# Kernel tuning notes

Measured on AMD Instinct MI355X. Metric: run time of the kernel, lower is better.

## Reference

```python
import jax, jax.numpy as jnp
import numpy as np

WINDOW_SIZES = (2, 4, 8)
HIDDEN = 32


def setup_inputs() -> dict:
    key = jax.random.key(0)
    ks = jax.random.split(key, 8)
    B, H, L = 4, 16, 1024
    S = len(WINDOW_SIZES)
    inp = {
        "attn_1": jax.random.uniform(ks[0], (B, H, L, L), dtype=jnp.float32),
        "attn_2": jax.random.uniform(ks[1], (B, H, L, L), dtype=jnp.float32),
        # gate MLP params, stacked over scales: Linear(8->32), Linear(32->16), Linear(16->1)
        "W1": jax.random.normal(ks[2], (S, HIDDEN, 8), dtype=jnp.float32) * 0.2,
        "b1": jnp.zeros((S, HIDDEN), dtype=jnp.float32),
        "W2": jax.random.normal(ks[3], (S, HIDDEN // 2, HIDDEN), dtype=jnp.float32) * 0.2,
        "b2": jnp.zeros((S, HIDDEN // 2), dtype=jnp.float32),
        "W3": jax.random.normal(ks[4], (S, 1, HIDDEN // 2), dtype=jnp.float32) * 0.2,
        "b3": jnp.zeros((S, 1), dtype=jnp.float32),
        "scale_weights": jnp.ones((S,), dtype=jnp.float32) / S,
    }
    return inp


def _window_stats(attn, ws):
    # attn: [B,H,L,L]; L % ws == 0 -> all windows are full-size (no edge merge)
    B, H, L, _ = attn.shape
    nw = L // ws
    x = attn.reshape(B, H, nw, ws, L)
    mean = x.mean(axis=-1).mean(axis=-1)                 # [B,H,nw]
    std = jnp.std(x, axis=-1, ddof=1).mean(axis=-1)      # torch.std is unbiased
    mx = x.max(axis=-1).mean(axis=-1)
    mn = x.min(axis=-1).mean(axis=-1)
    return jnp.stack([mean, std, mx, mn], axis=-1)        # [B,H,nw,4]


def reference(attn_1, attn_2, W1, b1, W2, b2, W3, b3, scale_weights):
    B, H, L, _ = attn_1.shape
    alphas = []
    for s, ws in enumerate(WINDOW_SIZES):
        g = jnp.concatenate([_window_stats(attn_1, ws), _window_stats(attn_2, ws)], axis=-1)  # [B,H,nw,8]
        h = jax.nn.relu(jnp.einsum('bhnf,of->bhno', g, W1[s]) + b1[s])
        h = jax.nn.relu(jnp.einsum('bhnf,of->bhno', h, W2[s]) + b2[s])
        a = jax.nn.sigmoid(jnp.einsum('bhnf,of->bhno', h, W3[s]) + b3[s])  # [B,H,nw,1]
        # expand per-window alpha to per-frame: repeat ws times (nw*ws == L)
        a_exp = jnp.repeat(a[..., 0], ws, axis=-1)[..., None]  # [B,H,L,1]
        alphas.append(a_exp)
    w = jax.nn.softmax(scale_weights)                     # all scales valid (max ws <= L)
    alpha_stacked = jnp.stack(alphas, axis=-1)            # [B,H,L,1,S]
    alpha_final = (alpha_stacked * w.reshape(1, 1, 1, 1, -1)).sum(axis=-1)
    return alpha_final
```

## Files before the change

kernel.cpp:

```cpp
#include <hip/hip_runtime.h>
#include <math.h>

#define L_DIM 1024
#define BH 64
#define ROWS_PER_TENSOR (BH * L_DIM)

typedef float floatx4 __attribute__((ext_vector_type(4)));

__global__ __launch_bounds__(256) void row_stats_kernel(
    const float* __restrict__ a1, const float* __restrict__ a2,
    float4* __restrict__ stats)
{
    const int wave = (blockIdx.x << 2) | (threadIdx.x >> 6);
    const int lane = threadIdx.x & 63;
    const int t = wave >> 16;
    const int r = wave & (ROWS_PER_TENSOR - 1);
    const float* __restrict__ src = t ? a2 : a1;
    const floatx4* __restrict__ rowp = (const floatx4*)(src + (size_t)r * L_DIM);

    float s = 0.f, sq = 0.f, mx = -INFINITY, mn = INFINITY;
#pragma unroll
    for (int c = 0; c < 4; ++c) {
        floatx4 v = __builtin_nontemporal_load(&rowp[(c << 6) + lane]);
        s  += v.x + v.y + v.z + v.w;
        sq += v.x * v.x + v.y * v.y + v.z * v.z + v.w * v.w;
        mx = fmaxf(mx, fmaxf(fmaxf(v.x, v.y), fmaxf(v.z, v.w)));
        mn = fminf(mn, fminf(fminf(v.x, v.y), fminf(v.z, v.w)));
    }
#pragma unroll
    for (int off = 32; off > 0; off >>= 1) {
        s  += __shfl_xor(s,  off, 64);
        sq += __shfl_xor(sq, off, 64);
        mx = fmaxf(mx, __shfl_xor(mx, off, 64));
        mn = fminf(mn, __shfl_xor(mn, off, 64));
    }
    if (lane == 0) {
        const float invL = 1.0f / (float)L_DIM;
        float mean = s * invL;
        float var  = (sq - s * s * invL) * (1.0f / (float)(L_DIM - 1));
        var = fmaxf(var, 0.f);
        float4 o;
        o.x = mean; o.y = sqrtf(var); o.z = mx; o.w = mn;
        stats[wave] = o;
    }
}

__global__ __launch_bounds__(256) void gate_kernel(
    const float4* __restrict__ stats,
    const float* __restrict__ W1, const float* __restrict__ b1,
    const float* __restrict__ W2, const float* __restrict__ b2,
    const float* __restrict__ W3, const float* __restrict__ b3,
    const float* __restrict__ sw,
    float* __restrict__ out)
{
    __shared__ float alpha[224];

    const int bh = blockIdx.x >> 2;
    const int l0 = (blockIdx.x & 3) << 8;
    const int tid = threadIdx.x;

    const float4* __restrict__ st1 = stats + (size_t)bh * L_DIM;
    const float4* __restrict__ st2 = stats + ROWS_PER_TENSOR + (size_t)bh * L_DIM;

    if (tid < 224) {
        int s, ws, r0;
        if (tid < 128)      { s = 0; ws = 2; r0 = l0 + (tid << 1); }
        else if (tid < 192) { s = 1; ws = 4; r0 = l0 + ((tid - 128) << 2); }
        else                { s = 2; ws = 8; r0 = l0 + ((tid - 192) << 3); }

        const int su = __builtin_amdgcn_readfirstlane(s);
        const float* __restrict__ W1p = W1 + su * 256;
        const float* __restrict__ b1p = b1 + su * 32;
        const float* __restrict__ W2p = W2 + su * 512;
        const float* __restrict__ b2p = b2 + su * 16;
        const float* __restrict__ W3p = W3 + su * 16;
        const float  b3v = b3[su];

        float g[8] = {0.f, 0.f, 0.f, 0.f, 0.f, 0.f, 0.f, 0.f};
        for (int j = 0; j < ws; ++j) {
            float4 v1 = st1[r0 + j];
            float4 v2 = st2[r0 + j];
            g[0] += v1.x; g[1] += v1.y; g[2] += v1.z; g[3] += v1.w;
            g[4] += v2.x; g[5] += v2.y; g[6] += v2.z; g[7] += v2.w;
        }
        const float inv = 1.0f / (float)ws;
#pragma unroll
        for (int k = 0; k < 8; ++k) g[k] *= inv;

        float h1[32];
#pragma unroll
        for (int o = 0; o < 32; ++o) {
            float acc = b1p[o];
#pragma unroll
            for (int f = 0; f < 8; ++f) acc += W1p[o * 8 + f] * g[f];
            h1[o] = fmaxf(acc, 0.f);
        }
        float h2[16];
#pragma unroll
        for (int o = 0; o < 16; ++o) {
            float acc = b2p[o];
#pragma unroll
            for (int f = 0; f < 32; ++f) acc += W2p[o * 32 + f] * h1[f];
            h2[o] = fmaxf(acc, 0.f);
        }
        float acc = b3v;
#pragma unroll
        for (int f = 0; f < 16; ++f) acc += W3p[f] * h2[f];

        alpha[tid] = 1.0f / (1.0f + expf(-acc));
    }
    __syncthreads();

    const float s0 = sw[0], s1 = sw[1], s2 = sw[2];
    const float m = fmaxf(s0, fmaxf(s1, s2));
    const float e0 = expf(s0 - m), e1 = expf(s1 - m), e2 = expf(s2 - m);
    const float einv = 1.0f / (e0 + e1 + e2);
    const float w0 = e0 * einv, w1 = e1 * einv, w2 = e2 * einv;

    out[(size_t)bh * L_DIM + l0 + tid] =
          w0 * alpha[tid >> 1]
        + w1 * alpha[128 + (tid >> 2)]
        + w2 * alpha[192 + (tid >> 3)];
}

extern "C" void kernel_launch(void* const* d_in, const int* in_sizes, int n_in,
                              void* d_out, int out_size, void* d_ws, size_t ws_size,
                              hipStream_t stream) {
    const float* attn1 = (const float*)d_in[0];
    const float* attn2 = (const float*)d_in[1];
    const float* W1 = (const float*)d_in[2];
    const float* b1 = (const float*)d_in[3];
    const float* W2 = (const float*)d_in[4];
    const float* b2 = (const float*)d_in[5];
    const float* W3 = (const float*)d_in[6];
    const float* b3 = (const float*)d_in[7];
    const float* sw = (const float*)d_in[8];
    float* out = (float*)d_out;

    float4* stats = (float4*)d_ws;

    const int n_rows = 2 * ROWS_PER_TENSOR;
    row_stats_kernel<<<n_rows / 4, 256, 0, stream>>>(attn1, attn2, stats);

    gate_kernel<<<BH * 4, 256, 0, stream>>>(stats, W1, b1, W2, b2, W3, b3, sw, out);
}
```

Measured before the change: 497.7 us.

## Fuse row-stats and gate MLP into one kernel per 8-row tile

Merges the row statistics kernel and the gate MLP kernel into a single launch. Each 512-thread block handles 8 rows of both tensors, with each wave reducing two rows, and keeps the stats in shared memory. Waves 0-2 then run the gate MLP for the windows that fall inside the tile. This removes the global stats round-trip and one kernel launch. The cost is that the MLP is now computed with only a few active lanes per wave and the block has to synchronize before it, which adds latency to a streaming kernel that is bandwidth-bound.

```diff
diff --git a/kernel.cpp b/kernel.cpp
--- a/kernel.cpp
+++ b/kernel.cpp
@@ -3,72 +3,77 @@
 
 #define L_DIM 1024
 #define BH 64
-#define ROWS_PER_TENSOR (BH * L_DIM)
 
 typedef float floatx4 __attribute__((ext_vector_type(4)));
 
-__global__ __launch_bounds__(256) void row_stats_kernel(
+__global__ __launch_bounds__(512) void fused_gate_kernel(
     const float* __restrict__ a1, const float* __restrict__ a2,
-    float4* __restrict__ stats)
-{
-    const int wave = (blockIdx.x << 2) | (threadIdx.x >> 6);
-    const int lane = threadIdx.x & 63;
-    const int t = wave >> 16;
-    const int r = wave & (ROWS_PER_TENSOR - 1);
-    const float* __restrict__ src = t ? a2 : a1;
-    const floatx4* __restrict__ rowp = (const floatx4*)(src + (size_t)r * L_DIM);
-
-    float s = 0.f, sq = 0.f, mx = -INFINITY, mn = INFINITY;
-#pragma unroll
-    for (int c = 0; c < 4; ++c) {
-        floatx4 v = __builtin_nontemporal_load(&rowp[(c << 6) + lane]);
-        s  += v.x + v.y + v.z + v.w;
-        sq += v.x * v.x + v.y * v.y + v.z * v.z + v.w * v.w;
-        mx = fmaxf(mx, fmaxf(fmaxf(v.x, v.y), fmaxf(v.z, v.w)));
-        mn = fminf(mn, fminf(fminf(v.x, v.y), fminf(v.z, v.w)));
-    }
-#pragma unroll
-    for (int off = 32; off > 0; off >>= 1) {
-        s  += __shfl_xor(s,  off, 64);
-        sq += __shfl_xor(sq, off, 64);
-        mx = fmaxf(mx, __shfl_xor(mx, off, 64));
-        mn = fminf(mn, __shfl_xor(mn, off, 64));
-    }
-    if (lane == 0) {
-        const float invL = 1.0f / (float)L_DIM;
-        float mean = s * invL;
-        float var  = (sq - s * s * invL) * (1.0f / (float)(L_DIM - 1));
-        var = fmaxf(var, 0.f);
-        float4 o;
-        o.x = mean; o.y = sqrtf(var); o.z = mx; o.w = mn;
-        stats[wave] = o;
-    }
-}
-
-__global__ __launch_bounds__(256) void gate_kernel(
-    const float4* __restrict__ stats,
     const float* __restrict__ W1, const float* __restrict__ b1,
     const float* __restrict__ W2, const float* __restrict__ b2,
     const float* __restrict__ W3, const float* __restrict__ b3,
     const float* __restrict__ sw,
     float* __restrict__ out)
 {
-    __shared__ float alpha[224];
+    __shared__ float4 sh_stats[16];
+    __shared__ float  sh_alpha[8];
 
-    const int bh = blockIdx.x >> 2;
-    const int l0 = (blockIdx.x & 3) << 8;
-    const int tid = threadIdx.x;
+    const int tid  = threadIdx.x;
+    const int w    = tid >> 6;
+    const int lane = tid & 63;
+    const int bh   = blockIdx.x >> 7;
+    const int row0 = (blockIdx.x & 127) << 3;
 
-    const float4* __restrict__ st1 = stats + (size_t)bh * L_DIM;
-    const float4* __restrict__ st2 = stats + ROWS_PER_TENSOR + (size_t)bh * L_DIM;
+    const int t  = w >> 2;
+    const int pr = (w & 3) << 1;
+    const float* __restrict__ src = t ? a2 : a1;
+    const floatx4* __restrict__ p =
+        (const floatx4*)(src + ((size_t)bh * L_DIM + row0 + pr) * L_DIM);
 
-    if (tid < 224) {
-        int s, ws, r0;
-        if (tid < 128)      { s = 0; ws = 2; r0 = l0 + (tid << 1); }
-        else if (tid < 192) { s = 1; ws = 4; r0 = l0 + ((tid - 128) << 2); }
-        else                { s = 2; ws = 8; r0 = l0 + ((tid - 192) << 3); }
+    float s0 = 0.f, q0 = 0.f, mx0 = -INFINITY, mn0 = INFINITY;
+    float s1 = 0.f, q1 = 0.f, mx1 = -INFINITY, mn1 = INFINITY;
+#pragma unroll
+    for (int c = 0; c < 4; ++c) {
+        floatx4 v = __builtin_nontemporal_load(&p[(c << 6) + lane]);
+        floatx4 u = __builtin_nontemporal_load(&p[256 + (c << 6) + lane]);
+        s0 += v.x + v.y + v.z + v.w;
+        q0 += v.x * v.x + v.y * v.y + v.z * v.z + v.w * v.w;
+        mx0 = fmaxf(mx0, fmaxf(fmaxf(v.x, v.y), fmaxf(v.z, v.w)));
+        mn0 = fminf(mn0, fminf(fminf(v.x, v.y), fminf(v.z, v.w)));
+        s1 += u.x + u.y + u.z + u.w;
+        q1 += u.x * u.x + u.y * u.y + u.z * u.z + u.w * u.w;
+        mx1 = fmaxf(mx1, fmaxf(fmaxf(u.x, u.y), fmaxf(u.z, u.w)));
+        mn1 = fminf(mn1, fminf(fminf(u.x, u.y), fminf(u.z, u.w)));
+    }
+#pragma unroll
+    for (int off = 32; off > 0; off >>= 1) {
+        s0 += __shfl_xor(s0, off, 64);  q0 += __shfl_xor(q0, off, 64);
+        mx0 = fmaxf(mx0, __shfl_xor(mx0, off, 64));
+        mn0 = fminf(mn0, __shfl_xor(mn0, off, 64));
+        s1 += __shfl_xor(s1, off, 64);  q1 += __shfl_xor(q1, off, 64);
+        mx1 = fmaxf(mx1, __shfl_xor(mx1, off, 64));
+        mn1 = fminf(mn1, __shfl_xor(mn1, off, 64));
+    }
+    if (lane == 0) {
+        const float invL  = 1.0f / (float)L_DIM;
+        const float invN1 = 1.0f / (float)(L_DIM - 1);
+        float4 o0, o1;
+        o0.x = s0 * invL;
+        o0.y = sqrtf(fmaxf((q0 - s0 * s0 * invL) * invN1, 0.f));
+        o0.z = mx0; o0.w = mn0;
+        o1.x = s1 * invL;
+        o1.y = sqrtf(fmaxf((q1 - s1 * s1 * invL) * invN1, 0.f));
+        o1.z = mx1; o1.w = mn1;
+        sh_stats[t * 8 + pr]     = o0;
+        sh_stats[t * 8 + pr + 1] = o1;
+    }
+    __syncthreads();
 
-        const int su = __builtin_amdgcn_readfirstlane(s);
+    if (w < 3) {
+        const int ws = 2 << w;
+        const int nw = 4 >> w;
+        const int wi = (lane < nw) ? lane : 0;
+
+        const int su = __builtin_amdgcn_readfirstlane(w);
         const float* __restrict__ W1p = W1 + su * 256;
         const float* __restrict__ b1p = b1 + su * 32;
         const float* __restrict__ W2p = W2 + su * 512;
@@ -78,8 +83,8 @@
 
         float g[8] = {0.f, 0.f, 0.f, 0.f, 0.f, 0.f, 0.f, 0.f};
         for (int j = 0; j < ws; ++j) {
-            float4 v1 = st1[r0 + j];
-            float4 v2 = st2[r0 + j];
+            float4 v1 = sh_stats[wi * ws + j];
+            float4 v2 = sh_stats[8 + wi * ws + j];
             g[0] += v1.x; g[1] += v1.y; g[2] += v1.z; g[3] += v1.w;
             g[4] += v2.x; g[5] += v2.y; g[6] += v2.z; g[7] += v2.w;
         }
@@ -107,20 +112,23 @@
 #pragma unroll
         for (int f = 0; f < 16; ++f) acc += W3p[f] * h2[f];
 
-        alpha[tid] = 1.0f / (1.0f + expf(-acc));
+        if (lane < nw) {
+            const int aoff = (w == 0) ? 0 : ((w == 1) ? 4 : 6);
+            sh_alpha[aoff + lane] = 1.0f / (1.0f + expf(-acc));
+        }
     }
     __syncthreads();
 
-    const float s0 = sw[0], s1 = sw[1], s2 = sw[2];
-    const float m = fmaxf(s0, fmaxf(s1, s2));
-    const float e0 = expf(s0 - m), e1 = expf(s1 - m), e2 = expf(s2 - m);
-    const float einv = 1.0f / (e0 + e1 + e2);
-    const float w0 = e0 * einv, w1 = e1 * einv, w2 = e2 * einv;
-
-    out[(size_t)bh * L_DIM + l0 + tid] =
-          w0 * alpha[tid >> 1]
-        + w1 * alpha[128 + (tid >> 2)]
-        + w2 * alpha[192 + (tid >> 3)];
+    if (tid < 8) {
+        const float x0 = sw[0], x1 = sw[1], x2 = sw[2];
+        const float m  = fmaxf(x0, fmaxf(x1, x2));
+        const float e0 = expf(x0 - m), e1 = expf(x1 - m), e2 = expf(x2 - m);
+        const float ei = 1.0f / (e0 + e1 + e2);
+        out[(size_t)bh * L_DIM + row0 + tid] =
+              (e0 * ei) * sh_alpha[tid >> 1]
+            + (e1 * ei) * sh_alpha[4 + (tid >> 2)]
+            + (e2 * ei) * sh_alpha[6];
+    }
 }
 
 extern "C" void kernel_launch(void* const* d_in, const int* in_sizes, int n_in,
@@ -137,10 +145,6 @@
     const float* sw = (const float*)d_in[8];
     float* out = (float*)d_out;
 
-    float4* stats = (float4*)d_ws;
-
-    const int n_rows = 2 * ROWS_PER_TENSOR;
-    row_stats_kernel<<<n_rows / 4, 256, 0, stream>>>(attn1, attn2, stats);
-
-    gate_kernel<<<BH * 4, 256, 0, stream>>>(stats, W1, b1, W2, b2, W3, b3, sw, out);
+    fused_gate_kernel<<<BH * 128, 512, 0, stream>>>(
+        attn1, attn2, W1, b1, W2, b2, W3, b3, sw, out);
 }
```

After: 531.4 us. 6.8% more time.
